# Kernel tuning notes

Hardware: AMD Instinct MI355X
Metric: run time of the kernel (lower is better)

Reference implementation:

```python
import jax, jax.numpy as jnp
import numpy as np

N_HEAD = 16

def apply_rope(t, cos, sin):
    # t: [B, H, T, hd]; cos/sin: [T, hd//2] -> broadcast [1,1,T,hd//2]
    hd = t.shape[-1]
    t1, t2 = t[..., : hd // 2], t[..., hd // 2 :]
    c = cos[None, None, :, :]
    s = sin[None, None, :, :]
    return jnp.concatenate([t1 * c - t2 * s, t1 * s + t2 * c], axis=-1)

def setup_inputs() -> dict:
    key = jax.random.key(0)
    k1, k2, k3, k4, k5 = jax.random.split(key, 5)
    B, T, C = 2, 2048, 2048
    hd = C // N_HEAD
    x = jax.random.normal(k1, (B, T, C), dtype=jnp.float32)
    cos = jax.random.uniform(k2, (T, hd // 2), dtype=jnp.float32)
    sin = jax.random.uniform(k3, (T, hd // 2), dtype=jnp.float32)
    W_attn = jax.random.normal(k4, (C, 3 * C), dtype=jnp.float32) * (1.0 / np.sqrt(C))
    W_proj = jax.random.normal(k5, (C, C), dtype=jnp.float32) * (1.0 / np.sqrt(C))
    return {"x": x, "cos": cos, "sin": sin, "W_attn": W_attn, "W_proj": W_proj}

def reference(x, cos, sin, W_attn, W_proj):
    B, T, C = x.shape
    hd = C // N_HEAD
    qkv = jnp.einsum("btc,cd->btd", x, W_attn)  # [B,T,3C]
    q, k, v = jnp.split(qkv, 3, axis=-1)
    # [B,T,C] -> [B,H,T,hd]
    def to_heads(t):
        return t.reshape(B, T, N_HEAD, hd).transpose(0, 2, 1, 3)
    q, k, v = to_heads(q), to_heads(k), to_heads(v)
    q = apply_rope(q, cos[:T], sin[:T])
    k = apply_rope(k, cos[:T], sin[:T])
    scale = 1.0 / np.sqrt(hd).astype(np.float32)
    scores = jnp.einsum("bhqd,bhkd->bhqk", q, k) * scale
    causal = jnp.tril(jnp.ones((T, T), dtype=bool))
    scores = jnp.where(causal[None, None], scores, jnp.finfo(scores.dtype).min)
    attn = jax.nn.softmax(scores, axis=-1)
    y = jnp.einsum("bhqk,bhkd->bhqd", attn, v)  # [B,H,T,hd]
    y = y.transpose(0, 2, 1, 3).reshape(B, T, C)
    return jnp.einsum("btc,cd->btd", y, W_proj)
```

## Files before the change

kernel.cpp:

```cpp
#include <hip/hip_runtime.h>
#include <stdint.h>

typedef unsigned short u16;
typedef __bf16 v8bf __attribute__((ext_vector_type(8)));
typedef float f32x4 __attribute__((ext_vector_type(4)));

#define MFMA16(a, b, c) __builtin_amdgcn_mfma_f32_16x16x32_bf16((a), (b), (c), 0, 0, 0)

typedef const __attribute__((address_space(1))) uint32_t* gp32;
typedef __attribute__((address_space(3))) uint32_t* lp32;
#define ASYNC16(g, l) __builtin_amdgcn_global_load_lds((gp32)(const void*)(g), (lp32)(void*)(l), 16, 0, 0)

__device__ __forceinline__ u16 f2bf(float f) {
  union { float f; uint32_t u; } v; v.f = f;
  uint32_t r = v.u + 0x7fffu + ((v.u >> 16) & 1u);
  return (u16)(r >> 16);
}
__device__ __forceinline__ float bf2f(u16 h) {
  union { uint32_t u; float f; } v; v.u = ((uint32_t)h) << 16;
  return v.f;
}

__device__ __forceinline__ int swK(int r, int lc) {
  return r * 128 + (((lc ^ (r & 7)) & 15) << 3);
}
__device__ __forceinline__ int swV(int r, int lc) {
  return r * 64 + (((lc ^ (r & 7)) & 7) << 3);
}

__global__ __launch_bounds__(256) void cast_x_kernel(const float* __restrict__ in,
                                                     u16* __restrict__ out) {
  int i = (blockIdx.x * 256 + threadIdx.x) * 8;
  float4 a = *(const float4*)(in + i);
  float4 b = *(const float4*)(in + i + 4);
  uint4 o;
  o.x = (uint32_t)f2bf(a.x) | ((uint32_t)f2bf(a.y) << 16);
  o.y = (uint32_t)f2bf(a.z) | ((uint32_t)f2bf(a.w) << 16);
  o.z = (uint32_t)f2bf(b.x) | ((uint32_t)f2bf(b.y) << 16);
  o.w = (uint32_t)f2bf(b.z) | ((uint32_t)f2bf(b.w) << 16);
  *(uint4*)(out + i) = o;
}

__global__ __launch_bounds__(256) void transpose_cast_kernel(const float* __restrict__ in,
                                                             u16* __restrict__ out,
                                                             int R, int Cc) {
  __shared__ u16 tile[32][34];
  int c0 = blockIdx.x * 32, r0 = blockIdx.y * 32;
  int tx = threadIdx.x, ty = threadIdx.y;
#pragma unroll
  for (int i = 0; i < 32; i += 8)
    tile[ty + i][tx] = f2bf(in[(size_t)(r0 + ty + i) * Cc + c0 + tx]);
  __syncthreads();
#pragma unroll
  for (int i = 0; i < 32; i += 8)
    out[(size_t)(c0 + ty + i) * R + r0 + tx] = tile[tx][ty + i];
}

template <typename OutT>
__global__ __launch_bounds__(256) void gemm_bt(const u16* __restrict__ A,
                                               const u16* __restrict__ Bt,
                                               OutT* __restrict__ C, int M, int N, int K) {
  __shared__ u16 As[128 * 64];
  __shared__ u16 Bs[128 * 64];
  int tid = threadIdx.x;
  int wave = tid >> 6, lane = tid & 63, quad = lane >> 4, l16 = lane & 15;
  int wr = wave >> 1, wc = wave & 1;
  int m0 = blockIdx.y * 128, n0 = blockIdx.x * 128;
  f32x4 acc[4][4] = {};
  int lrow = lane >> 3, lk = lane & 7;
  int lc = lk ^ lrow;
  const u16* Ab = A + (size_t)m0 * K;
  const u16* Bb = Bt + (size_t)n0 * K;

  for (int k0 = 0; k0 < K; k0 += 64) {
#pragma unroll
    for (int j = 0; j < 4; ++j) {
      int rbase = wave * 32 + j * 8;
      int row = rbase + lrow;
      ASYNC16(Ab + (size_t)row * K + k0 + lc * 8, &As[rbase * 64]);
      ASYNC16(Bb + (size_t)row * K + k0 + lc * 8, &Bs[rbase * 64]);
    }
    __syncthreads();
#pragma unroll
    for (int ks = 0; ks < 2; ++ks) {
      v8bf af[4], bfr[4];
#pragma unroll
      for (int t = 0; t < 4; ++t) {
        af[t]  = *(const v8bf*)&As[swV(wr * 64 + t * 16 + l16, ks * 4 + quad)];
        bfr[t] = *(const v8bf*)&Bs[swV(wc * 64 + t * 16 + l16, ks * 4 + quad)];
      }
#pragma unroll
      for (int mt = 0; mt < 4; ++mt)
#pragma unroll
        for (int nt = 0; nt < 4; ++nt)
          acc[mt][nt] = MFMA16(af[mt], bfr[nt], acc[mt][nt]);
    }
    __syncthreads();
  }
#pragma unroll
  for (int mt = 0; mt < 4; ++mt)
#pragma unroll
    for (int nt = 0; nt < 4; ++nt) {
      int row = m0 + wr * 64 + mt * 16 + quad * 4;
      int col = n0 + wc * 64 + nt * 16 + l16;
#pragma unroll
      for (int r = 0; r < 4; ++r) {
        float v = acc[mt][nt][r];
        if constexpr (sizeof(OutT) == 2)
          C[(size_t)(row + r) * N + col] = (OutT)f2bf(v);
        else
          C[(size_t)(row + r) * N + col] = v;
      }
    }
}

__global__ __launch_bounds__(256) void rope_repack(const u16* __restrict__ qkv,
                                                   const float* __restrict__ cosp,
                                                   const float* __restrict__ sinp,
                                                   u16* __restrict__ qh, u16* __restrict__ kh,
                                                   u16* __restrict__ vt) {
  __shared__ u16 tile[128 * 130];
  const int T = 2048, C3 = 6144;
  const float QSCL = 0.08838834764831845f * 1.4426950408889634f;
  int t0 = blockIdx.x * 128;
  int bh = blockIdx.y, b = bh >> 4, h = bh & 15;
  int tid = threadIdx.x;
#pragma unroll 2
  for (int i = 0; i < 32; ++i) {
    int e = i * 256 + tid;
    int tl = e >> 6, j = e & 63;
    int t = t0 + tl;
    size_t base = (size_t)(b * T + t) * C3 + h * 128;
    float c = cosp[t * 64 + j], s = sinp[t * 64 + j];
    float q1 = bf2f(qkv[base + j]),        q2 = bf2f(qkv[base + 64 + j]);
    float k1 = bf2f(qkv[base + 2048 + j]), k2 = bf2f(qkv[base + 2048 + 64 + j]);
    size_t o = ((size_t)bh * T + t) * 128;
    qh[o + j]      = f2bf((q1 * c - q2 * s) * QSCL);
    qh[o + 64 + j] = f2bf((q1 * s + q2 * c) * QSCL);
    kh[o + j]      = f2bf(k1 * c - k2 * s);
    kh[o + 64 + j] = f2bf(k1 * s + k2 * c);
  }
#pragma unroll 2
  for (int i = 0; i < 32; ++i) {
    int e = i * 256 + tid;
    int tl = e >> 6, dc = (e & 63) * 2;
    size_t base = (size_t)(b * T + t0 + tl) * C3 + 4096 + h * 128;
    *(uint32_t*)&tile[tl * 130 + dc] = *(const uint32_t*)&qkv[base + dc];
  }
  __syncthreads();
#pragma unroll 2
  for (int i = 0; i < 32; ++i) {
    int e = i * 256 + tid;
    int d = e >> 6, tp = (e & 63) * 2;
    uint32_t v = (uint32_t)tile[tp * 130 + d] | ((uint32_t)tile[(tp + 1) * 130 + d] << 16);
    *(uint32_t*)&vt[((size_t)bh * 128 + d) * T + t0 + tp] = v;
  }
}

__global__ __launch_bounds__(512) void flash_attn(const u16* __restrict__ qh,
                                                  const u16* __restrict__ kh,
                                                  const u16* __restrict__ vt,
                                                  u16* __restrict__ yh) {
  __shared__ u16 Ks[2][64 * 128];
  __shared__ u16 Vs[128 * 64];
  __shared__ u16 Pb[128 * 64];
  const int T = 2048, HD = 128;
  int tid = threadIdx.x;
  int wave = tid >> 6, lane = tid & 63, quad = lane >> 4, l16 = lane & 15;
  int bh = blockIdx.y, b = bh >> 4, h = bh & 15;
  const u16* qb = qh + (size_t)bh * T * HD;
  const u16* kb = kh + (size_t)bh * T * HD;
  const u16* vb = vt + (size_t)bh * HD * T;
  int krow_off = lane >> 4, kchunk = lane & 15;
  int vrow_off = lane >> 3, vchunk = lane & 7;

  for (int tp = 0; tp < 2; ++tp) {
    int qt = tp ? 15 - (int)blockIdx.x : (int)blockIdx.x;
    int q0 = qt * 128;
    int n_it = 2 * qt + 2;

    v8bf qf[4];
#pragma unroll
    for (int ks = 0; ks < 4; ++ks)
      qf[ks] = *(const v8bf*)&qb[(size_t)(q0 + wave * 16 + l16) * HD + ks * 32 + quad * 8];

    f32x4 acc[8] = {};
    float rs_p[4] = {};
    uint4 vreg[2];

#pragma unroll
    for (int j = 0; j < 2; ++j) {
      int rbase = wave * 8 + j * 4;
      int r = rbase + krow_off;
      int lc = kchunk ^ (r & 7);
      ASYNC16(kb + (size_t)r * HD + lc * 8, &Ks[0][rbase * 128]);
    }
#pragma unroll
    for (int j = 0; j < 2; ++j) {
      int row = wave * 16 + j * 8 + vrow_off;
      int lc = vchunk ^ (row & 7);
      vreg[j] = *(const uint4*)&vb[(size_t)row * T + lc * 8];
    }
    __syncthreads();
#pragma unroll
    for (int j = 0; j < 2; ++j) {
      int row = wave * 16 + j * 8 + vrow_off;
      *(uint4*)&Vs[row * 64 + vchunk * 8] = vreg[j];
    }

    for (int it = 0; it < n_it; ++it) {
      int c = it & 1;
      __syncthreads();

      if (it + 1 < n_it) {
        int kv0n = (it + 1) * 64;
#pragma unroll
        for (int j = 0; j < 2; ++j) {
          int rbase = wave * 8 + j * 4;
          int r = rbase + krow_off;
          int lc = kchunk ^ (r & 7);
          ASYNC16(kb + (size_t)(kv0n + r) * HD + lc * 8, &Ks[1 - c][rbase * 128]);
        }
#pragma unroll
        for (int j = 0; j < 2; ++j) {
          int row = wave * 16 + j * 8 + vrow_off;
          int lc = vchunk ^ (row & 7);
          vreg[j] = *(const uint4*)&vb[(size_t)row * T + kv0n + lc * 8];
        }
      }

      f32x4 s[4] = {};
#pragma unroll
      for (int ks = 0; ks < 4; ++ks)
#pragma unroll
        for (int nt = 0; nt < 4; ++nt) {
          v8bf kf = *(const v8bf*)&Ks[c][swK(nt * 16 + l16, ks * 4 + quad)];
          s[nt] = MFMA16(qf[ks], kf, s[nt]);
        }

      if (it >= 2 * qt) {
        int kv0 = it * 64;
#pragma unroll
        for (int r = 0; r < 4; ++r) {
          int row = q0 + wave * 16 + quad * 4 + r;
#pragma unroll
          for (int nt = 0; nt < 4; ++nt)
            if (kv0 + nt * 16 + l16 > row) s[nt][r] = -1e30f;
        }
      }

#pragma unroll
      for (int nt = 0; nt < 4; ++nt)
#pragma unroll
        for (int r = 0; r < 4; ++r) {
          float p = __builtin_exp2f(s[nt][r]);
          rs_p[r] += p;
          int row = wave * 16 + quad * 4 + r;
          int col = nt * 16 + l16;
          Pb[row * 64 + ((((col >> 3) ^ (row & 7)) & 7) << 3) + (col & 7)] = f2bf(p);
        }

#pragma unroll
      for (int ks = 0; ks < 2; ++ks) {
        v8bf pa = *(const v8bf*)&Pb[swV(wave * 16 + l16, ks * 4 + quad)];
#pragma unroll
        for (int dt = 0; dt < 8; ++dt) {
          v8bf vf = *(const v8bf*)&Vs[swV(dt * 16 + l16, ks * 4 + quad)];
          acc[dt] = MFMA16(pa, vf, acc[dt]);
        }
      }

      __syncthreads();

      if (it + 1 < n_it) {
#pragma unroll
        for (int j = 0; j < 2; ++j) {
          int row = wave * 16 + j * 8 + vrow_off;
          *(uint4*)&Vs[row * 64 + vchunk * 8] = vreg[j];
        }
      }
    }

#pragma unroll
    for (int r = 0; r < 4; ++r) {
      float rsv = rs_p[r];
      rsv += __shfl_xor(rsv, 1);
      rsv += __shfl_xor(rsv, 2);
      rsv += __shfl_xor(rsv, 4);
      rsv += __shfl_xor(rsv, 8);
      float inv = 1.f / rsv;
      int t = q0 + wave * 16 + quad * 4 + r;
#pragma unroll
      for (int dt = 0; dt < 8; ++dt)
        yh[(size_t)(b * T + t) * 2048 + h * 128 + dt * 16 + l16] = f2bf(acc[dt][r] * inv);
    }
  }
}

extern "C" void kernel_launch(void* const* d_in, const int* in_sizes, int n_in,
                              void* d_out, int out_size, void* d_ws, size_t ws_size,
                              hipStream_t stream) {
  const float* x    = (const float*)d_in[0];
  const float* cosp = (const float*)d_in[1];
  const float* sinp = (const float*)d_in[2];
  const float* Wa   = (const float*)d_in[3];
  const float* Wp   = (const float*)d_in[4];
  float* out = (float*)d_out;

  char* ws = (char*)d_ws;
  u16* xb  = (u16*)(ws);
  u16* WaT = (u16*)(ws + (size_t)(16 << 20));
  u16* WpT = (u16*)(ws + (size_t)(40 << 20));
  u16* qkv = (u16*)(ws + (size_t)(48 << 20));
  u16* qh  = (u16*)(ws + (size_t)(96 << 20));
  u16* kh  = (u16*)(ws + (size_t)(112 << 20));
  u16* vt  = (u16*)(ws + (size_t)(128 << 20));
  u16* yh  = (u16*)(ws + (size_t)(144 << 20));

  cast_x_kernel<<<4096, 256, 0, stream>>>(x, xb);
  transpose_cast_kernel<<<dim3(192, 64), dim3(32, 8), 0, stream>>>(Wa, WaT, 2048, 6144);
  transpose_cast_kernel<<<dim3(64, 64), dim3(32, 8), 0, stream>>>(Wp, WpT, 2048, 2048);
  gemm_bt<u16><<<dim3(48, 32), 256, 0, stream>>>(xb, WaT, qkv, 4096, 6144, 2048);
  rope_repack<<<dim3(16, 32), 256, 0, stream>>>(qkv, cosp, sinp, qh, kh, vt);
  flash_attn<<<dim3(8, 32), 512, 0, stream>>>(qh, kh, vt, yh);
  gemm_bt<float><<<dim3(16, 32), 256, 0, stream>>>(yh, WpT, out, 4096, 2048, 2048);
}
```

Measured before the change: 423.4 us.

## Triple-buffer GEMM with 128x256 tiles, 8 waves, and grid swizzle

```diff
diff --git a/kernel.cpp b/kernel.cpp
--- a/kernel.cpp
+++ b/kernel.cpp
@@ -57,46 +57,115 @@
 }
 
 template <typename OutT>
-__global__ __launch_bounds__(256) void gemm_bt(const u16* __restrict__ A,
+__global__ __launch_bounds__(512) void gemm_bt(const u16* __restrict__ A,
                                                const u16* __restrict__ Bt,
                                                OutT* __restrict__ C, int M, int N, int K) {
-  __shared__ u16 As[128 * 64];
-  __shared__ u16 Bs[128 * 64];
+  __shared__ u16 As[3][128 * 64];
+  __shared__ u16 Bs[3][256 * 64];
   int tid = threadIdx.x;
   int wave = tid >> 6, lane = tid & 63, quad = lane >> 4, l16 = lane & 15;
-  int wr = wave >> 1, wc = wave & 1;
-  int m0 = blockIdx.y * 128, n0 = blockIdx.x * 128;
+  int wr = wave >> 2, wc = wave & 3;
+  int nX = gridDim.x;
+  int nwg = nX * gridDim.y;
+  int id = blockIdx.y * nX + blockIdx.x;
+  int swz = (id & 7) * (nwg >> 3) + (id >> 3);
+  int bx = swz % nX, by = swz / nX;
+  int m0 = by * 128, n0 = bx * 256;
   f32x4 acc[4][4] = {};
-  int lrow = lane >> 3, lk = lane & 7;
-  int lc = lk ^ lrow;
+  int srow = tid >> 3;
+  int slot = tid & 7;
   const u16* Ab = A + (size_t)m0 * K;
   const u16* Bb = Bt + (size_t)n0 * K;
-
-  for (int k0 = 0; k0 < K; k0 += 64) {
+  int NT = K >> 6;
+
+#pragma unroll
+  for (int t = 0; t < 2; ++t) {
+#pragma unroll
+    for (int j = 0; j < 2; ++j) {
+      int row = j * 64 + srow;
+      int lc = slot ^ (row & 7);
+      ASYNC16(Ab + (size_t)row * K + t * 64 + lc * 8, &As[t][(j * 64 + (wave << 3)) * 64]);
+    }
 #pragma unroll
     for (int j = 0; j < 4; ++j) {
-      int rbase = wave * 32 + j * 8;
-      int row = rbase + lrow;
-      ASYNC16(Ab + (size_t)row * K + k0 + lc * 8, &As[rbase * 64]);
-      ASYNC16(Bb + (size_t)row * K + k0 + lc * 8, &Bs[rbase * 64]);
-    }
-    __syncthreads();
-#pragma unroll
-    for (int ks = 0; ks < 2; ++ks) {
-      v8bf af[4], bfr[4];
-#pragma unroll
-      for (int t = 0; t < 4; ++t) {
-        af[t]  = *(const v8bf*)&As[swV(wr * 64 + t * 16 + l16, ks * 4 + quad)];
-        bfr[t] = *(const v8bf*)&Bs[swV(wc * 64 + t * 16 + l16, ks * 4 + quad)];
-      }
-#pragma unroll
-      for (int mt = 0; mt < 4; ++mt)
+      int row = j * 64 + srow;
+      int lc = slot ^ (row & 7);
+      ASYNC16(Bb + (size_t)row * K + t * 64 + lc * 8, &Bs[t][(j * 64 + (wave << 3)) * 64]);
+    }
+  }
+
+  for (int t = 0; t < NT; ++t) {
+    int cur = t % 3;
+    int pre = (t + 2) % 3;
+    bool do_pre = (t + 2) < NT;
+    asm volatile("s_waitcnt lgkmcnt(0)" ::: "memory");
+    if (t + 1 < NT)
+      asm volatile("s_waitcnt vmcnt(6)" ::: "memory");
+    else
+      asm volatile("s_waitcnt vmcnt(0)" ::: "memory");
+    __builtin_amdgcn_s_barrier();
+
+    if (do_pre) {
+#pragma unroll
+      for (int j = 0; j < 2; ++j) {
+        int row = j * 64 + srow;
+        int lc = slot ^ (row & 7);
+        ASYNC16(Ab + (size_t)row * K + (t + 2) * 64 + lc * 8,
+                &As[pre][(j * 64 + (wave << 3)) * 64]);
+      }
+      {
+        int row = srow;
+        int lc = slot ^ (row & 7);
+        ASYNC16(Bb + (size_t)row * K + (t + 2) * 64 + lc * 8, &Bs[pre][(wave << 3) * 64]);
+      }
+    }
+    v8bf afr[2][2], bfr[4][2];
+#pragma unroll
+    for (int x = 0; x < 2; ++x)
+#pragma unroll
+      for (int ks = 0; ks < 2; ++ks)
+        afr[x][ks] = *(const v8bf*)&As[cur][swV(wr * 64 + x * 16 + l16, ks * 4 + quad)];
+#pragma unroll
+    for (int nt = 0; nt < 4; ++nt)
+#pragma unroll
+      for (int ks = 0; ks < 2; ++ks)
+        bfr[nt][ks] = *(const v8bf*)&Bs[cur][swV(wc * 64 + nt * 16 + l16, ks * 4 + quad)];
+    __builtin_amdgcn_s_setprio(1);
+#pragma unroll
+    for (int ks = 0; ks < 2; ++ks)
+#pragma unroll
+      for (int x = 0; x < 2; ++x)
 #pragma unroll
         for (int nt = 0; nt < 4; ++nt)
-          acc[mt][nt] = MFMA16(af[mt], bfr[nt], acc[mt][nt]);
-    }
-    __syncthreads();
-  }
+          acc[x][nt] = MFMA16(afr[x][ks], bfr[nt][ks], acc[x][nt]);
+    __builtin_amdgcn_s_setprio(0);
+    __builtin_amdgcn_s_barrier();
+
+    if (do_pre) {
+#pragma unroll
+      for (int j = 1; j < 4; ++j) {
+        int row = j * 64 + srow;
+        int lc = slot ^ (row & 7);
+        ASYNC16(Bb + (size_t)row * K + (t + 2) * 64 + lc * 8,
+                &Bs[pre][(j * 64 + (wave << 3)) * 64]);
+      }
+    }
+#pragma unroll
+    for (int x = 0; x < 2; ++x)
+#pragma unroll
+      for (int ks = 0; ks < 2; ++ks)
+        afr[x][ks] = *(const v8bf*)&As[cur][swV(wr * 64 + (2 + x) * 16 + l16, ks * 4 + quad)];
+    __builtin_amdgcn_s_setprio(1);
+#pragma unroll
+    for (int ks = 0; ks < 2; ++ks)
+#pragma unroll
+      for (int x = 0; x < 2; ++x)
+#pragma unroll
+        for (int nt = 0; nt < 4; ++nt)
+          acc[2 + x][nt] = MFMA16(afr[x][ks], bfr[nt][ks], acc[2 + x][nt]);
+    __builtin_amdgcn_s_setprio(0);
+  }
+
 #pragma unroll
   for (int mt = 0; mt < 4; ++mt)
 #pragma unroll
@@ -320,8 +389,8 @@
   cast_x_kernel<<<4096, 256, 0, stream>>>(x, xb);
   transpose_cast_kernel<<<dim3(192, 64), dim3(32, 8), 0, stream>>>(Wa, WaT, 2048, 6144);
   transpose_cast_kernel<<<dim3(64, 64), dim3(32, 8), 0, stream>>>(Wp, WpT, 2048, 2048);
-  gemm_bt<u16><<<dim3(48, 32), 256, 0, stream>>>(xb, WaT, qkv, 4096, 6144, 2048);
+  gemm_bt<u16><<<dim3(24, 32), 512, 0, stream>>>(xb, WaT, qkv, 4096, 6144, 2048);
   rope_repack<<<dim3(16, 32), 256, 0, stream>>>(qkv, cosp, sinp, qh, kh, vt);
   flash_attn<<<dim3(8, 32), 512, 0, stream>>>(qh, kh, vt, yh);
-  gemm_bt<float><<<dim3(16, 32), 256, 0, stream>>>(yh, WpT, out, 4096, 2048, 2048);
-}
+  gemm_bt<float><<<dim3(8, 32), 512, 0, stream>>>(yh, WpT, out, 4096, 2048, 2048);
+}
```

After: 507.1 us. +19.8%, slower.

## Add 256x256 eight-phase pipelined GEMM for the QKV projection

Applied to the files above, without the earlier changes.

```diff
diff --git a/kernel.cpp b/kernel.cpp
--- a/kernel.cpp
+++ b/kernel.cpp
@@ -112,6 +112,155 @@
           C[(size_t)(row + r) * N + col] = v;
       }
     }
+}
+
+template <typename OutT>
+__global__ __launch_bounds__(512, 2) void gemm_bt_8ph(const u16* __restrict__ A,
+                                                      const u16* __restrict__ Bt,
+                                                      OutT* __restrict__ C,
+                                                      int M, int N, int K) {
+  __shared__ u16 As[2][256 * 64];
+  __shared__ u16 Bs[2][256 * 64];
+  int tid = threadIdx.x;
+  int wave = tid >> 6, lane = tid & 63, quad = lane >> 4, l16 = lane & 15;
+  int wr = wave >> 2, wc = wave & 3;
+  int m0 = blockIdx.y * 256, n0 = blockIdx.x * 256;
+  const u16* Ab = A + (size_t)m0 * K;
+  const u16* Bb = Bt + (size_t)n0 * K;
+  int srow = tid >> 3;
+  int lc8 = (tid & 7) ^ (srow & 7);
+  int NI = K >> 7;
+  f32x4 acc[8][4] = {};
+  v8bf af[4][2], bf[4][2];
+
+#define STG(gbase, lbase, half, kt)                                                   \
+  do {                                                                                \
+    _Pragma("unroll") for (int r_ = 0; r_ < 2; ++r_) {                                \
+      int row_ = (half) * 128 + r_ * 64 + srow;                                       \
+      ASYNC16(gbase + (size_t)row_ * K + (kt) * 64 + lc8 * 8,                         \
+              &lbase[((half) * 128 + r_ * 64 + (wave << 3)) * 64]);                   \
+    }                                                                                 \
+  } while (0)
+
+#define LDA4(d, i0)                                                                   \
+  do {                                                                                \
+    _Pragma("unroll") for (int x_ = 0; x_ < 4; ++x_)                                  \
+    _Pragma("unroll") for (int k_ = 0; k_ < 2; ++k_)                                  \
+      af[x_][k_] = *(const v8bf*)&As[d][swV(wr * 128 + ((i0) + x_) * 16 + l16,        \
+                                            k_ * 4 + quad)];                          \
+  } while (0)
+
+#define LDB4(d)                                                                       \
+  do {                                                                                \
+    _Pragma("unroll") for (int x_ = 0; x_ < 4; ++x_)                                  \
+    _Pragma("unroll") for (int k_ = 0; k_ < 2; ++k_)                                  \
+      bf[x_][k_] = *(const v8bf*)&Bs[d][swV(wc * 64 + x_ * 16 + l16, k_ * 4 + quad)]; \
+  } while (0)
+
+#define MM16(i0, j0)                                                                  \
+  do {                                                                                \
+    __builtin_amdgcn_s_setprio(1);                                                    \
+    _Pragma("unroll") for (int k_ = 0; k_ < 2; ++k_)                                  \
+    _Pragma("unroll") for (int x_ = 0; x_ < 4; ++x_)                                  \
+    _Pragma("unroll") for (int j_ = 0; j_ < 2; ++j_)                                  \
+      acc[(i0) + x_][(j0) + j_] =                                                     \
+          MFMA16(af[x_][k_], bf[(j0) + j_][k_], acc[(i0) + x_][(j0) + j_]);           \
+    __builtin_amdgcn_s_setprio(0);                                                    \
+  } while (0)
+
+#define BAR() __builtin_amdgcn_s_barrier()
+#define LGK0() asm volatile("s_waitcnt lgkmcnt(0)" ::: "memory")
+#define LGK8() asm volatile("s_waitcnt lgkmcnt(8)" ::: "memory")
+
+  STG(Ab, As[0], 0, 0);
+  STG(Ab, As[0], 1, 0);
+  STG(Bb, Bs[0], 0, 0);
+  STG(Bb, Bs[0], 1, 0);
+  STG(Bb, Bs[1], 0, 1);
+  STG(Bb, Bs[1], 1, 1);
+  STG(Ab, As[1], 0, 1);
+  asm volatile("s_waitcnt vmcnt(6)" ::: "memory");
+  BAR();
+
+  for (int i = 0; i < NI; ++i) {
+    int t2 = 2 * i + 2, t3 = 2 * i + 3;
+    bool s2 = t2 < (K >> 6), s3 = t3 < (K >> 6);
+
+    LDA4(0, 0);
+    LDB4(0);
+    STG(Ab, As[1], 1, 2 * i + 1);
+    LGK8();
+    BAR();
+    LGK0();
+    MM16(0, 0);
+    BAR();
+    if (s2) STG(Bb, Bs[0], 0, t2);
+    BAR();
+    MM16(0, 2);
+    BAR();
+    LDA4(0, 4);
+    if (s2) STG(Bb, Bs[0], 1, t2);
+    BAR();
+    LGK0();
+    MM16(4, 0);
+    BAR();
+    if (s2) STG(Ab, As[0], 0, t2);
+    BAR();
+    MM16(4, 2);
+    if (s2)
+      asm volatile("s_waitcnt vmcnt(6)" ::: "memory");
+    else
+      asm volatile("s_waitcnt vmcnt(0)" ::: "memory");
+    BAR();
+    LDA4(1, 0);
+    LDB4(1);
+    if (s2) STG(Ab, As[0], 1, t2);
+    LGK8();
+    BAR();
+    LGK0();
+    MM16(0, 0);
+    BAR();
+    if (s3) STG(Bb, Bs[1], 0, t3);
+    BAR();
+    MM16(0, 2);
+    BAR();
+    LDA4(1, 4);
+    if (s3) STG(Bb, Bs[1], 1, t3);
+    BAR();
+    LGK0();
+    MM16(4, 0);
+    BAR();
+    if (s3) STG(Ab, As[1], 0, t3);
+    BAR();
+    MM16(4, 2);
+    if (i + 1 < NI) {
+      asm volatile("s_waitcnt vmcnt(6)" ::: "memory");
+      BAR();
+    }
+  }
+
+#pragma unroll
+  for (int mt = 0; mt < 8; ++mt)
+#pragma unroll
+    for (int nt = 0; nt < 4; ++nt) {
+      int row = m0 + wr * 128 + mt * 16 + quad * 4;
+      int col = n0 + wc * 64 + nt * 16 + l16;
+#pragma unroll
+      for (int r = 0; r < 4; ++r) {
+        float v = acc[mt][nt][r];
+        if constexpr (sizeof(OutT) == 2)
+          C[(size_t)(row + r) * N + col] = (OutT)f2bf(v);
+        else
+          C[(size_t)(row + r) * N + col] = v;
+      }
+    }
+#undef STG
+#undef LDA4
+#undef LDB4
+#undef MM16
+#undef BAR
+#undef LGK0
+#undef LGK8
 }
 
 __global__ __launch_bounds__(256) void rope_repack(const u16* __restrict__ qkv,
@@ -320,7 +469,7 @@
   cast_x_kernel<<<4096, 256, 0, stream>>>(x, xb);
   transpose_cast_kernel<<<dim3(192, 64), dim3(32, 8), 0, stream>>>(Wa, WaT, 2048, 6144);
   transpose_cast_kernel<<<dim3(64, 64), dim3(32, 8), 0, stream>>>(Wp, WpT, 2048, 2048);
-  gemm_bt<u16><<<dim3(48, 32), 256, 0, stream>>>(xb, WaT, qkv, 4096, 6144, 2048);
+  gemm_bt_8ph<u16><<<dim3(24, 16), 512, 0, stream>>>(xb, WaT, qkv, 4096, 6144, 2048);
   rope_repack<<<dim3(16, 32), 256, 0, stream>>>(qkv, cosp, sinp, qh, kh, vt);
   flash_attn<<<dim3(8, 32), 512, 0, stream>>>(qh, kh, vt, yh);
   gemm_bt<float><<<dim3(16, 32), 256, 0, stream>>>(yh, WpT, out, 4096, 2048, 2048);
```

New measurement: 434.0 us. +2.5%, slower.

## Fuse prep casts into one launch and double-buffer V tile in attention

Applied to the files above, without the earlier changes.

```diff
diff --git a/kernel.cpp b/kernel.cpp
--- a/kernel.cpp
+++ b/kernel.cpp
@@ -28,25 +28,12 @@
   return r * 64 + (((lc ^ (r & 7)) & 7) << 3);
 }
 
-__global__ __launch_bounds__(256) void cast_x_kernel(const float* __restrict__ in,
-                                                     u16* __restrict__ out) {
-  int i = (blockIdx.x * 256 + threadIdx.x) * 8;
-  float4 a = *(const float4*)(in + i);
-  float4 b = *(const float4*)(in + i + 4);
-  uint4 o;
-  o.x = (uint32_t)f2bf(a.x) | ((uint32_t)f2bf(a.y) << 16);
-  o.y = (uint32_t)f2bf(a.z) | ((uint32_t)f2bf(a.w) << 16);
-  o.z = (uint32_t)f2bf(b.x) | ((uint32_t)f2bf(b.y) << 16);
-  o.w = (uint32_t)f2bf(b.z) | ((uint32_t)f2bf(b.w) << 16);
-  *(uint4*)(out + i) = o;
-}
-
-__global__ __launch_bounds__(256) void transpose_cast_kernel(const float* __restrict__ in,
-                                                             u16* __restrict__ out,
-                                                             int R, int Cc) {
-  __shared__ u16 tile[32][34];
-  int c0 = blockIdx.x * 32, r0 = blockIdx.y * 32;
-  int tx = threadIdx.x, ty = threadIdx.y;
+__device__ __forceinline__ void transpose_tile(const float* __restrict__ in,
+                                               u16* __restrict__ out, int R, int Cc,
+                                               int bx, int by, int tid,
+                                               u16 (*tile)[34]) {
+  int c0 = bx * 32, r0 = by * 32;
+  int tx = tid & 31, ty = tid >> 5;
 #pragma unroll
   for (int i = 0; i < 32; i += 8)
     tile[ty + i][tx] = f2bf(in[(size_t)(r0 + ty + i) * Cc + c0 + tx]);
@@ -54,6 +41,34 @@
 #pragma unroll
   for (int i = 0; i < 32; i += 8)
     out[(size_t)(c0 + ty + i) * R + r0 + tx] = tile[tx][ty + i];
+}
+
+__global__ __launch_bounds__(256) void prep_kernel(const float* __restrict__ x,
+                                                   u16* __restrict__ xb,
+                                                   const float* __restrict__ Wa,
+                                                   u16* __restrict__ WaT,
+                                                   const float* __restrict__ Wp,
+                                                   u16* __restrict__ WpT) {
+  __shared__ u16 tile[32][34];
+  int bid = blockIdx.x;
+  int tid = threadIdx.x;
+  if (bid < 4096) {
+    int i = (bid * 256 + tid) * 8;
+    float4 a = *(const float4*)(x + i);
+    float4 b = *(const float4*)(x + i + 4);
+    uint4 o;
+    o.x = (uint32_t)f2bf(a.x) | ((uint32_t)f2bf(a.y) << 16);
+    o.y = (uint32_t)f2bf(a.z) | ((uint32_t)f2bf(a.w) << 16);
+    o.z = (uint32_t)f2bf(b.x) | ((uint32_t)f2bf(b.y) << 16);
+    o.w = (uint32_t)f2bf(b.z) | ((uint32_t)f2bf(b.w) << 16);
+    *(uint4*)(xb + i) = o;
+  } else if (bid < 4096 + 12288) {
+    int t = bid - 4096;
+    transpose_tile(Wa, WaT, 2048, 6144, t % 192, t / 192, tid, tile);
+  } else {
+    int t = bid - 16384;
+    transpose_tile(Wp, WpT, 2048, 2048, t & 63, t >> 6, tid, tile);
+  }
 }
 
 template <typename OutT>
@@ -162,7 +177,7 @@
                                                   const u16* __restrict__ vt,
                                                   u16* __restrict__ yh) {
   __shared__ u16 Ks[2][64 * 128];
-  __shared__ u16 Vs[128 * 64];
+  __shared__ u16 Vs[2][128 * 64];
   __shared__ u16 Pb[128 * 64];
   const int T = 2048, HD = 128;
   int tid = threadIdx.x;
@@ -201,16 +216,15 @@
       int lc = vchunk ^ (row & 7);
       vreg[j] = *(const uint4*)&vb[(size_t)row * T + lc * 8];
     }
-    __syncthreads();
 #pragma unroll
     for (int j = 0; j < 2; ++j) {
       int row = wave * 16 + j * 8 + vrow_off;
-      *(uint4*)&Vs[row * 64 + vchunk * 8] = vreg[j];
-    }
+      *(uint4*)&Vs[0][row * 64 + vchunk * 8] = vreg[j];
+    }
+    __syncthreads();
 
     for (int it = 0; it < n_it; ++it) {
       int c = it & 1;
-      __syncthreads();
 
       if (it + 1 < n_it) {
         int kv0n = (it + 1) * 64;
@@ -265,20 +279,20 @@
         v8bf pa = *(const v8bf*)&Pb[swV(wave * 16 + l16, ks * 4 + quad)];
 #pragma unroll
         for (int dt = 0; dt < 8; ++dt) {
-          v8bf vf = *(const v8bf*)&Vs[swV(dt * 16 + l16, ks * 4 + quad)];
+          v8bf vf = *(const v8bf*)&Vs[c][swV(dt * 16 + l16, ks * 4 + quad)];
           acc[dt] = MFMA16(pa, vf, acc[dt]);
         }
       }
-
-      __syncthreads();
 
       if (it + 1 < n_it) {
 #pragma unroll
         for (int j = 0; j < 2; ++j) {
           int row = wave * 16 + j * 8 + vrow_off;
-          *(uint4*)&Vs[row * 64 + vchunk * 8] = vreg[j];
-        }
-      }
+          *(uint4*)&Vs[1 - c][row * 64 + vchunk * 8] = vreg[j];
+        }
+      }
+
+      __syncthreads();
     }
 
 #pragma unroll
@@ -317,9 +331,7 @@
   u16* vt  = (u16*)(ws + (size_t)(128 << 20));
   u16* yh  = (u16*)(ws + (size_t)(144 << 20));
 
-  cast_x_kernel<<<4096, 256, 0, stream>>>(x, xb);
-  transpose_cast_kernel<<<dim3(192, 64), dim3(32, 8), 0, stream>>>(Wa, WaT, 2048, 6144);
-  transpose_cast_kernel<<<dim3(64, 64), dim3(32, 8), 0, stream>>>(Wp, WpT, 2048, 2048);
+  prep_kernel<<<20480, 256, 0, stream>>>(x, xb, Wa, WaT, Wp, WpT);
   gemm_bt<u16><<<dim3(48, 32), 256, 0, stream>>>(xb, WaT, qkv, 4096, 6144, 2048);
   rope_repack<<<dim3(16, 32), 256, 0, stream>>>(qkv, cosp, sinp, qh, kh, vt);
   flash_attn<<<dim3(8, 32), 512, 0, stream>>>(qh, kh, vt, yh);
```

After: 407.2 us. 3.8% less time.
